# Kernel optimization log

Measured on AMD Instinct MI355X. Metric: run time of the kernel, lower is better.

The kernel has to match this reference:

```python
import jax, jax.numpy as jnp
import numpy as np

T, B, E, H = 2048, 2, 1024, 16

def setup_inputs() -> dict:
    rng = jax.random.key(0)
    ks = jax.random.split(rng, 7)
    s = 0.02
    return {
        "query": jax.random.normal(ks[0], (T, B, E), jnp.float32),
        "key": jax.random.normal(ks[1], (T, B, E), jnp.float32),
        "value": jax.random.normal(ks[2], (T, B, E), jnp.float32),
        "in_proj_weight": jax.random.normal(ks[3], (3 * E, E), jnp.float32) * s,
        "in_proj_bias": jax.random.normal(ks[4], (3 * E,), jnp.float32) * s,
        "out_proj_weight": jax.random.normal(ks[5], (E, E), jnp.float32) * s,
        "out_proj_bias": jax.random.normal(ks[6], (E,), jnp.float32) * s,
    }

def reference(query, key, value, in_proj_weight, in_proj_bias, out_proj_weight, out_proj_bias):
    tgt_len, bsz, embed_dim = query.shape
    num_heads = H
    head_dim = embed_dim // num_heads
    scaling = head_dim ** -0.5
    wq, wk, wv = jnp.split(in_proj_weight, 3, axis=0)
    bq, bk, bv = jnp.split(in_proj_bias, 3, axis=0)
    # projections: F.linear(x, W, b) = x @ W.T + b
    q = (query @ wq.T + bq) * scaling          # (T, B, E)
    k = key @ wk.T + bk                        # (S, B, E)
    v = value @ wv.T + bv                      # (S, B, E)
    # (len, B, E) -> (B*H, len, head_dim), matching torch view+transpose
    def to_heads(x):
        L = x.shape[0]
        return x.reshape(L, bsz * num_heads, head_dim).transpose(1, 0, 2)
    q, k, v = to_heads(q), to_heads(k), to_heads(v)
    scores = jnp.einsum('bqd,bkd->bqk', q, k)  # (B*H, T, S)
    attn = jax.nn.softmax(scores, axis=-1)
    out = jnp.einsum('bqk,bkd->bqd', attn, v)  # (B*H, T, head_dim)
    out = out.transpose(1, 0, 2).reshape(tgt_len, bsz, embed_dim)
    out = out @ out_proj_weight.T + out_proj_bias
    return out
```

## Files before the change

### kernel.cpp

```cpp
#include <hip/hip_runtime.h>
#include <cstdint>
#include <cstddef>

#define QSCALE 0.18033688011112042f

typedef __attribute__((ext_vector_type(8))) short bf16x8;
typedef __attribute__((ext_vector_type(4))) float f32x4;

#define MFMA(a, b, c) __builtin_amdgcn_mfma_f32_16x16x32_bf16(a, b, c, 0, 0, 0)

typedef union { unsigned int u[4]; bf16x8 b; } pku;

__device__ __forceinline__ unsigned short cvt_bf16(float x) {
  union { float f; unsigned int u; } v;
  v.f = x;
  unsigned int r = v.u + 0x7FFFu + ((v.u >> 16) & 1u);
  return (unsigned short)(r >> 16);
}

__device__ __forceinline__ void gll16(const void* g, void* l) {
  __builtin_amdgcn_global_load_lds(
      (const __attribute__((address_space(1))) unsigned int*)g,
      (__attribute__((address_space(3))) unsigned int*)l, 16, 0, 0);
}

__device__ __forceinline__ float fast_exp2(float x) {
#if __has_builtin(__builtin_amdgcn_exp2f)
  return __builtin_amdgcn_exp2f(x);
#else
  float r; asm("v_exp_f32 %0, %1" : "=v"(r) : "v"(x)); return r;
#endif
}

__device__ __forceinline__ unsigned int pack_bf16(float lo, float hi) {
  union { float f; unsigned int u; } a, b;
  a.f = lo; b.f = hi;
  return __builtin_amdgcn_perm(b.u + 0x8000u, a.u + 0x8000u, 0x07060302u);
}

__global__ void cvt_all(const float* __restrict__ q,
                        const float* __restrict__ k,
                        const float* __restrict__ v,
                        const float* __restrict__ ipw,
                        const float* __restrict__ opw,
                        unsigned short* __restrict__ dst) {
  const size_t i = ((size_t)blockIdx.x * 256 + threadIdx.x) * 8;
  const float* src;
  float scale = 1.0f;
  if (i < 4194304) src = q + i;
  else if (i < 8388608) src = k + (i - 4194304);
  else if (i < 12582912) src = v + (i - 8388608);
  else {
    const size_t w = i - 12582912;
    if (w < 3145728) { src = ipw + w; if (w < 1048576) scale = QSCALE; }
    else src = opw + (w - 3145728);
  }
  float4 a = *(const float4*)src;
  float4 b = *(const float4*)(src + 4);
  uint4 o;
  o.x = cvt_bf16(a.x * scale) | ((unsigned int)cvt_bf16(a.y * scale) << 16);
  o.y = cvt_bf16(a.z * scale) | ((unsigned int)cvt_bf16(a.w * scale) << 16);
  o.z = cvt_bf16(b.x * scale) | ((unsigned int)cvt_bf16(b.y * scale) << 16);
  o.w = cvt_bf16(b.z * scale) | ((unsigned int)cvt_bf16(b.w * scale) << 16);
  *(uint4*)(dst + i) = o;
}

__global__ __launch_bounds__(256, 3) void gemm_qkv(
    const unsigned short* __restrict__ X,
    const unsigned short* __restrict__ W,
    const float* __restrict__ bias,
    unsigned short* __restrict__ Qh,
    unsigned short* __restrict__ Kh,
    unsigned short* __restrict__ Vt)
{
  __shared__ unsigned short As[128 * 64];
  __shared__ unsigned short Bs[128 * 64];
  const int tid = threadIdx.x;
  const int wave = tid >> 6, lane = tid & 63;
  const int quad = lane >> 4, l16 = lane & 15;
  const int flat = blockIdx.x + (blockIdx.y << 3) + (blockIdx.z << 8);
  const int nf = (flat & 7) * 96 + (flat >> 3);
  const int z = nf >> 8;
  const int m0 = ((nf >> 3) & 31) * 128;
  const int n0 = (nf & 7) * 128;
  const unsigned short* Ab = X + (size_t)z * 4194304 + (size_t)m0 * 1024;
  const unsigned short* Bb = W + ((size_t)z * 1024 + n0) * 1024;
  const int wr = (wave >> 1) * 64, wc = (wave & 1) * 64;

  const f32x4 z4 = {0.f, 0.f, 0.f, 0.f};
  f32x4 acc[4][4];
#pragma unroll
  for (int i = 0; i < 4; ++i)
#pragma unroll
    for (int j = 0; j < 4; ++j) acc[i][j] = z4;

  for (int k0 = 0; k0 < 1024; k0 += 64) {
    __syncthreads();
#pragma unroll
    for (int j = 0; j < 4; ++j) {
      const int c = j * 256 + tid;
      const int row = c >> 3, pc = c & 7;
      const int kc = pc ^ (row & 7);
      gll16(Ab + (size_t)row * 1024 + k0 + kc * 8, &As[c * 8]);
      gll16(Bb + (size_t)row * 1024 + k0 + kc * 8, &Bs[c * 8]);
    }
    __syncthreads();
#pragma unroll
    for (int kk = 0; kk < 2; ++kk) {
      bf16x8 af[4], bfr[4];
#pragma unroll
      for (int rt = 0; rt < 4; ++rt) {
        const int row = wr + rt * 16 + l16;
        af[rt] = *(const bf16x8*)&As[row * 64 + ((kk * 4 + quad) ^ (row & 7)) * 8];
      }
#pragma unroll
      for (int ct = 0; ct < 4; ++ct) {
        const int row = wc + ct * 16 + l16;
        bfr[ct] = *(const bf16x8*)&Bs[row * 64 + ((kk * 4 + quad) ^ (row & 7)) * 8];
      }
#pragma unroll
      for (int rt = 0; rt < 4; ++rt)
#pragma unroll
        for (int ct = 0; ct < 4; ++ct)
          acc[rt][ct] = MFMA(af[rt], bfr[ct], acc[rt][ct]);
    }
  }

#pragma unroll
  for (int rt = 0; rt < 4; ++rt)
#pragma unroll
    for (int ct = 0; ct < 4; ++ct) {
      const int gn = n0 + wc + ct * 16 + l16;
      float bv = bias[z * 1024 + gn];
      if (z == 0) bv *= QSCALE;
      const int h = gn >> 6, d = gn & 63;
#pragma unroll
      for (int r = 0; r < 4; ++r) {
        const int gm = m0 + wr + rt * 16 + quad * 4 + r;
        const int t = gm >> 1, b = gm & 1;
        const int bh = b * 16 + h;
        const unsigned short o = cvt_bf16(acc[rt][ct][r] + bv);
        if (z == 0)      Qh[((size_t)bh * 2048 + t) * 64 + d] = o;
        else if (z == 1) Kh[((size_t)bh * 2048 + t) * 64 + d] = o;
        else {
          const int w32 = t & 31;
          const int tp = (t & ~31) | (((w32 >> 2) & 3) << 3) | ((w32 >> 4) << 2) | (w32 & 3);
          Vt[((size_t)bh * 64 + d) * 2048 + tp] = o;
        }
      }
    }
}

__global__ __launch_bounds__(256, 4) void attn(
    const unsigned short* __restrict__ Qh,
    const unsigned short* __restrict__ Kh,
    const unsigned short* __restrict__ Vt,
    unsigned short* __restrict__ O)
{
  __shared__ unsigned short Ks[128 * 64];
  __shared__ unsigned short Vs[64 * 128];
  const int tid = threadIdx.x;
  const int wave = tid >> 6, lane = tid & 63;
  const int quad = lane >> 4, l16 = lane & 15;
  const int flat = blockIdx.x + (blockIdx.y << 5);
  const int nf = (flat & 7) * 128 + (flat >> 3);
  const int qt = nf & 31, bh = nf >> 5;
  const unsigned short* Qb = Qh + ((size_t)bh * 2048 + qt * 64 + wave * 16) * 64;
  const unsigned short* Kb = Kh + (size_t)bh * 2048 * 64;
  const unsigned short* Vb = Vt + (size_t)bh * 64 * 2048;

  bf16x8 qf[2];
#pragma unroll
  for (int kk = 0; kk < 2; ++kk)
    qf[kk] = *(const bf16x8*)(Qb + (size_t)l16 * 64 + kk * 32 + quad * 8);

  const unsigned short* kp[4];
  const unsigned short* vp[4];
  unsigned short* kl[4];
  unsigned short* vl[4];
#pragma unroll
  for (int j = 0; j < 4; ++j) {
    const int c = wave * 256 + j * 64 + lane;
    const int r = c >> 3, cc = c & 7;
    kp[j] = Kb + (size_t)r * 64 + (cc ^ (r & 7)) * 8;
    kl[j] = &Ks[c * 8];
    const int r2 = c >> 4, cc2 = c & 15;
    vp[j] = Vb + (size_t)r2 * 2048 + (cc2 ^ (r2 & 15)) * 8;
    vl[j] = &Vs[c * 8];
  }

  pku ones;
  ones.u[0] = ones.u[1] = ones.u[2] = ones.u[3] = 0x3F803F80u;

  const f32x4 z4 = {0.f, 0.f, 0.f, 0.f};
  f32x4 oacc[4];
  f32x4 lacc = z4;
#pragma unroll
  for (int c = 0; c < 4; ++c) oacc[c] = z4;

#pragma unroll 1
  for (int it = 0; it < 16; ++it) {
    __syncthreads();
#pragma unroll
    for (int j = 0; j < 4; ++j) {
      gll16(kp[j], kl[j]);
      gll16(vp[j], vl[j]);
      kp[j] += 128 * 64;
      vp[j] += 128;
    }
    __syncthreads();

    unsigned int pkl_[8], pkh_[8];
#pragma unroll
    for (int ct = 0; ct < 8; ++ct) {
      f32x4 sv = z4;
#pragma unroll
      for (int kk = 0; kk < 2; ++kk) {
        const int R = ct * 16 + l16;
        const int phys = (kk * 4 + quad) ^ (R & 7);
        const bf16x8 kfr = *(const bf16x8*)&Ks[R * 64 + phys * 8];
        sv = MFMA(kfr, qf[kk], sv);
      }
      f32x4 p;
#pragma unroll
      for (int r = 0; r < 4; ++r) p[r] = fast_exp2(sv[r]);
      pkl_[ct] = pack_bf16(p[0], p[1]);
      pkh_[ct] = pack_bf16(p[2], p[3]);
    }

#pragma unroll
    for (int kk2 = 0; kk2 < 4; ++kk2) {
      pku a0;
      a0.u[0] = pkl_[kk2 * 2];     a0.u[1] = pkh_[kk2 * 2];
      a0.u[2] = pkl_[kk2 * 2 + 1]; a0.u[3] = pkh_[kk2 * 2 + 1];
#pragma unroll
      for (int ctd = 0; ctd < 4; ++ctd) {
        const int R = ctd * 16 + l16;
        const int phys = (kk2 * 4 + quad) ^ (R & 15);
        const bf16x8 vv = *(const bf16x8*)&Vs[R * 128 + phys * 8];
        oacc[ctd] = MFMA(a0.b, vv, oacc[ctd]);
      }
      lacc = MFMA(a0.b, ones.b, lacc);
    }
  }

  const int b = bh >> 4, h = bh & 15;
#pragma unroll
  for (int r = 0; r < 4; ++r) {
    const float inv = 1.0f / lacc[r];
    const int t = qt * 64 + wave * 16 + quad * 4 + r;
#pragma unroll
    for (int ctd = 0; ctd < 4; ++ctd) {
      const int col = h * 64 + ctd * 16 + l16;
      O[((size_t)t * 2 + b) * 1024 + col] = cvt_bf16(oacc[ctd][r] * inv);
    }
  }
}

__global__ __launch_bounds__(256, 4) void gemm_out(
    const unsigned short* __restrict__ A,
    const unsigned short* __restrict__ W,
    const float* __restrict__ bias,
    float* __restrict__ out)
{
  __shared__ unsigned short As[128 * 64];
  __shared__ unsigned short Bs[64 * 64];
  const int tid = threadIdx.x;
  const int wave = tid >> 6, lane = tid & 63;
  const int quad = lane >> 4, l16 = lane & 15;
  const int flat = blockIdx.x + (blockIdx.y << 4);
  const int nf = (flat & 7) * 64 + (flat >> 3);
  const int m0 = (nf >> 4) * 128;
  const int n0 = (nf & 15) * 64;
  const unsigned short* Ab = A + (size_t)m0 * 1024;
  const unsigned short* Bb = W + (size_t)n0 * 1024;
  const int wr = (wave >> 1) * 64, wc = (wave & 1) * 32;

  const f32x4 z4 = {0.f, 0.f, 0.f, 0.f};
  f32x4 acc[4][2];
#pragma unroll
  for (int i = 0; i < 4; ++i)
#pragma unroll
    for (int j = 0; j < 2; ++j) acc[i][j] = z4;

  for (int k0 = 0; k0 < 1024; k0 += 64) {
    __syncthreads();
#pragma unroll
    for (int j = 0; j < 4; ++j) {
      const int c = j * 256 + tid;
      const int row = c >> 3, pc = c & 7;
      const int kc = pc ^ (row & 7);
      gll16(Ab + (size_t)row * 1024 + k0 + kc * 8, &As[c * 8]);
    }
#pragma unroll
    for (int j = 0; j < 2; ++j) {
      const int c = j * 256 + tid;
      const int row = c >> 3, pc = c & 7;
      const int kc = pc ^ (row & 7);
      gll16(Bb + (size_t)row * 1024 + k0 + kc * 8, &Bs[c * 8]);
    }
    __syncthreads();
#pragma unroll
    for (int kk = 0; kk < 2; ++kk) {
      bf16x8 af[4], bfr[2];
#pragma unroll
      for (int rt = 0; rt < 4; ++rt) {
        const int row = wr + rt * 16 + l16;
        af[rt] = *(const bf16x8*)&As[row * 64 + ((kk * 4 + quad) ^ (row & 7)) * 8];
      }
#pragma unroll
      for (int ct = 0; ct < 2; ++ct) {
        const int row = wc + ct * 16 + l16;
        bfr[ct] = *(const bf16x8*)&Bs[row * 64 + ((kk * 4 + quad) ^ (row & 7)) * 8];
      }
#pragma unroll
      for (int rt = 0; rt < 4; ++rt)
#pragma unroll
        for (int ct = 0; ct < 2; ++ct)
          acc[rt][ct] = MFMA(af[rt], bfr[ct], acc[rt][ct]);
    }
  }

#pragma unroll
  for (int rt = 0; rt < 4; ++rt)
#pragma unroll
    for (int ct = 0; ct < 2; ++ct) {
      const int gn = n0 + wc + ct * 16 + l16;
      const float bv = bias[gn];
#pragma unroll
      for (int r = 0; r < 4; ++r) {
        const int gm = m0 + wr + rt * 16 + quad * 4 + r;
        out[(size_t)gm * 1024 + gn] = acc[rt][ct][r] + bv;
      }
    }
}

extern "C" void kernel_launch(void* const* d_in, const int* in_sizes, int n_in,
                              void* d_out, int out_size, void* d_ws, size_t ws_size,
                              hipStream_t stream) {
  const float* q   = (const float*)d_in[0];
  const float* k   = (const float*)d_in[1];
  const float* v   = (const float*)d_in[2];
  const float* ipw = (const float*)d_in[3];
  const float* ipb = (const float*)d_in[4];
  const float* opw = (const float*)d_in[5];
  const float* opb = (const float*)d_in[6];

  unsigned short* ws = (unsigned short*)d_ws;
  unsigned short* X  = ws;
  unsigned short* Wb = ws + 12582912;
  unsigned short* Wo = ws + 15728640;
  unsigned short* Qh = ws + 16777216;
  unsigned short* Kh = ws + 20971520;
  unsigned short* Vx = ws + 25165824;
  unsigned short* Oa = ws + 29360128;

  cvt_all<<<dim3(8192), 256, 0, stream>>>(q, k, v, ipw, opw, ws);
  gemm_qkv<<<dim3(8, 32, 3), 256, 0, stream>>>(X, Wb, ipb, Qh, Kh, Vx);
  attn<<<dim3(32, 32), 256, 0, stream>>>(Qh, Kh, Vx, Oa);
  gemm_out<<<dim3(16, 32), 256, 0, stream>>>(Oa, Wo, opb, (float*)d_out);
}
```

Before: 215.0 us.

## Process four query sub-tiles per wave in attention to reuse K/V loads

Each attention block now covers 256 query rows instead of 64: every wave holds four 16-row Q fragments and reuses each K and V fragment read from shared memory across all four. The grid shrinks from 1024 to 256 blocks, and launch bounds drop to one block per CU to leave room for the larger accumulator set. This cuts global K/V traffic and LDS reads per query row, at the cost of far more registers, lower occupancy, and only 256 blocks to spread across the GPU. The softmax still does no max subtraction, same as before.

```diff
diff --git a/kernel.cpp b/kernel.cpp
--- a/kernel.cpp
+++ b/kernel.cpp
@@ -151,7 +151,7 @@
     }
 }
 
-__global__ __launch_bounds__(256, 4) void attn(
+__global__ __launch_bounds__(256, 1) void attn(
     const unsigned short* __restrict__ Qh,
     const unsigned short* __restrict__ Kh,
     const unsigned short* __restrict__ Vt,
@@ -162,17 +162,19 @@
   const int tid = threadIdx.x;
   const int wave = tid >> 6, lane = tid & 63;
   const int quad = lane >> 4, l16 = lane & 15;
-  const int flat = blockIdx.x + (blockIdx.y << 5);
-  const int nf = (flat & 7) * 128 + (flat >> 3);
-  const int qt = nf & 31, bh = nf >> 5;
-  const unsigned short* Qb = Qh + ((size_t)bh * 2048 + qt * 64 + wave * 16) * 64;
+  const int flat = blockIdx.x + (blockIdx.y << 3);
+  const int nf = (flat & 7) * 32 + (flat >> 3);
+  const int qt = nf & 7, bh = nf >> 3;
+  const unsigned short* Qb = Qh + ((size_t)bh * 2048 + qt * 256 + wave * 64) * 64;
   const unsigned short* Kb = Kh + (size_t)bh * 2048 * 64;
   const unsigned short* Vb = Vt + (size_t)bh * 64 * 2048;
 
-  bf16x8 qf[2];
-#pragma unroll
-  for (int kk = 0; kk < 2; ++kk)
-    qf[kk] = *(const bf16x8*)(Qb + (size_t)l16 * 64 + kk * 32 + quad * 8);
+  bf16x8 qf[4][2];
+#pragma unroll
+  for (int g = 0; g < 4; ++g)
+#pragma unroll
+    for (int kk = 0; kk < 2; ++kk)
+      qf[g][kk] = *(const bf16x8*)(Qb + (size_t)(g * 16 + l16) * 64 + kk * 32 + quad * 8);
 
   const unsigned short* kp[4];
   const unsigned short* vp[4];
@@ -193,10 +195,12 @@
   ones.u[0] = ones.u[1] = ones.u[2] = ones.u[3] = 0x3F803F80u;
 
   const f32x4 z4 = {0.f, 0.f, 0.f, 0.f};
-  f32x4 oacc[4];
-  f32x4 lacc = z4;
-#pragma unroll
-  for (int c = 0; c < 4; ++c) oacc[c] = z4;
+  f32x4 oacc[4][4];
+  f32x4 lacc[4] = {z4, z4, z4, z4};
+#pragma unroll
+  for (int g = 0; g < 4; ++g)
+#pragma unroll
+    for (int c = 0; c < 4; ++c) oacc[g][c] = z4;
 
 #pragma unroll 1
   for (int it = 0; it < 16; ++it) {
@@ -210,51 +214,65 @@
     }
     __syncthreads();
 
-    unsigned int pkl_[8], pkh_[8];
-#pragma unroll
-    for (int ct = 0; ct < 8; ++ct) {
-      f32x4 sv = z4;
-#pragma unroll
-      for (int kk = 0; kk < 2; ++kk) {
+#pragma unroll
+    for (int jj = 0; jj < 4; ++jj) {
+      unsigned int pk0[4][2], pk1[4][2];
+#pragma unroll
+      for (int half = 0; half < 2; ++half) {
+        const int ct = jj * 2 + half;
         const int R = ct * 16 + l16;
-        const int phys = (kk * 4 + quad) ^ (R & 7);
-        const bf16x8 kfr = *(const bf16x8*)&Ks[R * 64 + phys * 8];
-        sv = MFMA(kfr, qf[kk], sv);
-      }
-      f32x4 p;
-#pragma unroll
-      for (int r = 0; r < 4; ++r) p[r] = fast_exp2(sv[r]);
-      pkl_[ct] = pack_bf16(p[0], p[1]);
-      pkh_[ct] = pack_bf16(p[2], p[3]);
-    }
-
-#pragma unroll
-    for (int kk2 = 0; kk2 < 4; ++kk2) {
-      pku a0;
-      a0.u[0] = pkl_[kk2 * 2];     a0.u[1] = pkh_[kk2 * 2];
-      a0.u[2] = pkl_[kk2 * 2 + 1]; a0.u[3] = pkh_[kk2 * 2 + 1];
+        bf16x8 kfr[2];
+#pragma unroll
+        for (int kk = 0; kk < 2; ++kk)
+          kfr[kk] = *(const bf16x8*)&Ks[R * 64 + (((kk * 4 + quad) ^ (R & 7))) * 8];
+#pragma unroll
+        for (int g = 0; g < 4; ++g) {
+          f32x4 sv = z4;
+          sv = MFMA(kfr[0], qf[g][0], sv);
+          sv = MFMA(kfr[1], qf[g][1], sv);
+          f32x4 p;
+#pragma unroll
+          for (int r = 0; r < 4; ++r) p[r] = fast_exp2(sv[r]);
+          pk0[g][half] = pack_bf16(p[0], p[1]);
+          pk1[g][half] = pack_bf16(p[2], p[3]);
+        }
+      }
 #pragma unroll
       for (int ctd = 0; ctd < 4; ++ctd) {
         const int R = ctd * 16 + l16;
-        const int phys = (kk2 * 4 + quad) ^ (R & 15);
+        const int phys = (jj * 4 + quad) ^ (R & 15);
         const bf16x8 vv = *(const bf16x8*)&Vs[R * 128 + phys * 8];
-        oacc[ctd] = MFMA(a0.b, vv, oacc[ctd]);
-      }
-      lacc = MFMA(a0.b, ones.b, lacc);
+#pragma unroll
+        for (int g = 0; g < 4; ++g) {
+          pku a;
+          a.u[0] = pk0[g][0]; a.u[1] = pk1[g][0];
+          a.u[2] = pk0[g][1]; a.u[3] = pk1[g][1];
+          oacc[g][ctd] = MFMA(a.b, vv, oacc[g][ctd]);
+        }
+      }
+#pragma unroll
+      for (int g = 0; g < 4; ++g) {
+        pku a;
+        a.u[0] = pk0[g][0]; a.u[1] = pk1[g][0];
+        a.u[2] = pk0[g][1]; a.u[3] = pk1[g][1];
+        lacc[g] = MFMA(a.b, ones.b, lacc[g]);
+      }
     }
   }
 
   const int b = bh >> 4, h = bh & 15;
 #pragma unroll
-  for (int r = 0; r < 4; ++r) {
-    const float inv = 1.0f / lacc[r];
-    const int t = qt * 64 + wave * 16 + quad * 4 + r;
-#pragma unroll
-    for (int ctd = 0; ctd < 4; ++ctd) {
-      const int col = h * 64 + ctd * 16 + l16;
-      O[((size_t)t * 2 + b) * 1024 + col] = cvt_bf16(oacc[ctd][r] * inv);
-    }
-  }
+  for (int g = 0; g < 4; ++g)
+#pragma unroll
+    for (int r = 0; r < 4; ++r) {
+      const float inv = 1.0f / lacc[g][r];
+      const int t = qt * 256 + wave * 64 + g * 16 + quad * 4 + r;
+#pragma unroll
+      for (int ctd = 0; ctd < 4; ++ctd) {
+        const int col = h * 64 + ctd * 16 + l16;
+        O[((size_t)t * 2 + b) * 1024 + col] = cvt_bf16(oacc[g][ctd][r] * inv);
+      }
+    }
 }
 
 __global__ __launch_bounds__(256, 4) void gemm_out(
@@ -357,6 +375,6 @@
 
   cvt_all<<<dim3(8192), 256, 0, stream>>>(q, k, v, ipw, opw, ws);
   gemm_qkv<<<dim3(8, 32, 3), 256, 0, stream>>>(X, Wb, ipb, Qh, Kh, Vx);
-  attn<<<dim3(32, 32), 256, 0, stream>>>(Qh, Kh, Vx, Oa);
+  attn<<<dim3(8, 32), 256, 0, stream>>>(Qh, Kh, Vx, Oa);
   gemm_out<<<dim3(16, 32), 256, 0, stream>>>(Oa, Wo, opb, (float*)d_out);
 }
```

Result: no change. 217.7 us (+1.3%).
